# Performance work log

Measured on AMD Instinct MI355X. Metric: run time of the kernel, lower is better.

Reference implementation:

```python
import jax, jax.numpy as jnp
import numpy as np

B, S, D, H = 4, 2048, 1024, 16
HD = D // H  # head_size = 64
SCALE = HD ** -0.5


def setup_inputs() -> dict:
    key = jax.random.key(0)
    k1, k2, k3 = jax.random.split(key, 3)
    hidden_states = jax.random.normal(k1, (B, S, D), dtype=jnp.float32)
    W_qkv = jax.random.normal(k2, (D, 3 * D), dtype=jnp.float32) * 0.02
    W_out = jax.random.normal(k3, (D, D), dtype=jnp.float32) * 0.02
    return {"hidden_states": hidden_states, "W_qkv": W_qkv, "W_out": W_out}


def reference(hidden_states, W_qkv, W_out):
    b, s, d = hidden_states.shape
    qkv = hidden_states @ W_qkv                      # [b, s, 3d]
    q, k, v = jnp.split(qkv, 3, axis=-1)
    # [b, s, d] -> [b, H, s, hd]
    q = q.reshape(b, s, H, HD).transpose(0, 2, 1, 3)
    k = k.reshape(b, s, H, HD).transpose(0, 2, 1, 3)
    v = v.reshape(b, s, H, HD).transpose(0, 2, 1, 3)
    scores = jnp.einsum("bhqd,bhkd->bhqk", q, k) * SCALE  # [b, H, s, s]
    probs = jax.nn.softmax(scores, axis=-1)
    ctx = jnp.einsum("bhqk,bhkd->bhqd", probs, v)         # [b, H, s, hd]
    ctx = ctx.transpose(0, 2, 1, 3).reshape(b, s, d)
    out = ctx @ W_out
    return out
```

## Files before the change

kernel.cpp:

```cpp
#include <hip/hip_runtime.h>

typedef __attribute__((ext_vector_type(8))) __bf16 bf8;
typedef __attribute__((ext_vector_type(4))) float f4;
typedef __attribute__((ext_vector_type(8))) unsigned short us8;
typedef __attribute__((ext_vector_type(4))) unsigned short us4;
typedef __attribute__((ext_vector_type(4))) unsigned int u32x4;
typedef __attribute__((ext_vector_type(2))) unsigned int u32x2;

#define MFMA16(a, b, c) __builtin_amdgcn_mfma_f32_16x16x32_bf16((a), (b), (c), 0, 0, 0)
#define GLOAD16(gp, lp)                                                        \
  __builtin_amdgcn_global_load_lds(                                            \
      (const __attribute__((address_space(1))) void*)(gp),                     \
      (__attribute__((address_space(3))) void*)(lp), 16, 0, 0)

__device__ __forceinline__ unsigned short f2bf(float f) {
  unsigned u = __builtin_bit_cast(unsigned, f);
  u += 0x7FFFu + ((u >> 16) & 1u);
  return (unsigned short)(u >> 16);
}

__device__ __forceinline__ float fexp2(float x) {
  float r;
  asm("v_exp_f32 %0, %1" : "=v"(r) : "v"(x));
  return r;
}

__device__ __forceinline__ unsigned cvtpk(float a, float b) {
  unsigned r;
  asm("v_cvt_pk_bf16_f32 %0, %1, %2" : "=v"(r) : "v"(a), "v"(b));
  return r;
}

__global__ __launch_bounds__(256) void c_cast(const float* __restrict__ in,
                                              unsigned short* __restrict__ out) {
  int i = blockIdx.x * 256 + threadIdx.x;
  const float4* p = reinterpret_cast<const float4*>(in) + (size_t)i * 2;
  float4 a = p[0], b = p[1];
  us8 o;
  o[0] = f2bf(a.x); o[1] = f2bf(a.y); o[2] = f2bf(a.z); o[3] = f2bf(a.w);
  o[4] = f2bf(b.x); o[5] = f2bf(b.y); o[6] = f2bf(b.z); o[7] = f2bf(b.w);
  *reinterpret_cast<us8*>(&out[(size_t)i * 8]) = o;
}

__global__ __launch_bounds__(256) void c_trans(const float* __restrict__ in,
                                               unsigned short* __restrict__ out,
                                               int R, int C) {
  __shared__ float T[64][65];
  const int t = threadIdx.x;
  const int c0 = blockIdx.x * 64, r0 = blockIdx.y * 64;
  const int tr = t >> 4, tc = (t & 15) * 4;
#pragma unroll
  for (int i = 0; i < 4; ++i) {
    int r = tr + i * 16;
    float4 v = *reinterpret_cast<const float4*>(&in[(size_t)(r0 + r) * C + c0 + tc]);
    T[r][tc] = v.x; T[r][tc + 1] = v.y; T[r][tc + 2] = v.z; T[r][tc + 3] = v.w;
  }
  __syncthreads();
#pragma unroll
  for (int i = 0; i < 4; ++i) {
    int c = tr + i * 16;
    us4 o;
    o[0] = f2bf(T[tc + 0][c]); o[1] = f2bf(T[tc + 1][c]);
    o[2] = f2bf(T[tc + 2][c]); o[3] = f2bf(T[tc + 3][c]);
    *reinterpret_cast<us4*>(&out[(size_t)(c0 + c) * R + r0 + tc]) = o;
  }
}

__global__ __launch_bounds__(256) void k_qkv(const unsigned short* __restrict__ A,
                                             const unsigned short* __restrict__ Bt,
                                             unsigned short* __restrict__ Qo,
                                             unsigned short* __restrict__ Ko,
                                             unsigned short* __restrict__ Vo) {
  __shared__ unsigned short As[2][128 * 32];
  __shared__ unsigned short Bs[2][128 * 32];
  const int t = threadIdx.x;
  const int lane = t & 63, wid = t >> 6;
  const int wr = wid >> 1, wc = wid & 1;
  const int cl = lane & 15, kr8 = (lane >> 4) << 3;
  const int id = blockIdx.x;
  const int s = (id & 7) * 192 + (id >> 3);
  const int m0 = (s / 24) << 7, n0 = (s % 24) << 7;

  f4 acc[4][4];
#pragma unroll
  for (int i = 0; i < 4; ++i)
#pragma unroll
    for (int j = 0; j < 4; ++j) acc[i][j] = (f4){0.f, 0.f, 0.f, 0.f};

  auto STAGE = [&](int buf, int kt) {
    int k0 = kt << 5;
#pragma unroll
    for (int it = 0; it < 2; ++it) {
      int c = t + (it << 8);
      int wb = (t & 192) + (it << 8);
      GLOAD16(A + (size_t)(m0 + (c >> 2)) * 1024 + k0 + ((c & 3) << 3),
              (char*)As[buf] + (size_t)wb * 16);
      GLOAD16(Bt + (size_t)(n0 + (c >> 2)) * 1024 + k0 + ((c & 3) << 3),
              (char*)Bs[buf] + (size_t)wb * 16);
    }
  };

  STAGE(0, 0);
  __syncthreads();
  for (int kt = 0; kt < 32; ++kt) {
    int cur = kt & 1;
    if (kt < 31) STAGE(cur ^ 1, kt + 1);
    const unsigned short* as = As[cur];
    const unsigned short* bs = Bs[cur];
    bf8 af[4], bfr[4];
#pragma unroll
    for (int mi = 0; mi < 4; ++mi)
      af[mi] = *reinterpret_cast<const bf8*>(&as[(wr * 64 + mi * 16 + cl) * 32 + kr8]);
#pragma unroll
    for (int ni = 0; ni < 4; ++ni)
      bfr[ni] = *reinterpret_cast<const bf8*>(&bs[(wc * 64 + ni * 16 + cl) * 32 + kr8]);
#pragma unroll
    for (int mi = 0; mi < 4; ++mi)
#pragma unroll
      for (int ni = 0; ni < 4; ++ni)
        acc[mi][ni] = MFMA16(af[mi], bfr[ni], acc[mi][ni]);
    __syncthreads();
  }

#pragma unroll
  for (int mi = 0; mi < 4; ++mi) {
#pragma unroll
    for (int ni = 0; ni < 4; ++ni) {
      int gcol = n0 + wc * 64 + ni * 16 + cl;
      int grow0 = m0 + wr * 64 + mi * 16 + ((lane >> 4) << 2);
      int b = grow0 >> 11, s0 = grow0 & 2047;
      if (gcol < 1024) {
        int h = gcol >> 6, hd = gcol & 63;
#pragma unroll
        for (int r = 0; r < 4; ++r)
          Qo[((size_t)(b * 16 + h) * 2048 + s0 + r) * 64 + hd] =
              f2bf(acc[mi][ni][r] * 0.18033688011112042f);
      } else if (gcol < 2048) {
        int cc = gcol - 1024;
        int h = cc >> 6, hd = cc & 63;
#pragma unroll
        for (int r = 0; r < 4; ++r)
          Ko[((size_t)(b * 16 + h) * 2048 + s0 + r) * 64 + hd] = f2bf(acc[mi][ni][r]);
      } else {
        int cc = gcol - 2048;
        int h = cc >> 6, hd = cc & 63;
        us4 o;
        o[0] = f2bf(acc[mi][ni][0]); o[1] = f2bf(acc[mi][ni][1]);
        o[2] = f2bf(acc[mi][ni][2]); o[3] = f2bf(acc[mi][ni][3]);
        *reinterpret_cast<us4*>(&Vo[((size_t)(b * 16 + h) * 64 + hd) * 2048 + s0]) = o;
      }
    }
  }
}

__global__ __launch_bounds__(512) void k_attn(const unsigned short* __restrict__ Q,
                                              const unsigned short* __restrict__ K,
                                              const unsigned short* __restrict__ Vt,
                                              unsigned short* __restrict__ Ctx) {
  __shared__ __align__(16) unsigned short SMEM[2][2][64 * 64];
  __shared__ float RedS[128];
  const int t = threadIdx.x;
  const int lane = t & 63, wid = t >> 6;
  const int cl = lane & 15, g = lane >> 4;
  const int qg = wid >> 1, kg = wid & 1;
  const int id = blockIdx.x;
  const int sw = (id & 7) * 128 + (id >> 3);
  const int bh = sw >> 4, qb = sw & 15;
  const int b = bh >> 4, h = bh & 15;
  const int q0 = qb << 7;
  const size_t base = (size_t)bh * (2048 * 64);

  bf8 qf[2][2];
#pragma unroll
  for (int qi = 0; qi < 2; ++qi) {
    int qrow = q0 + qg * 32 + qi * 16 + cl;
    qf[qi][0] = *reinterpret_cast<const bf8*>(&Q[base + (size_t)qrow * 64 + (g << 3)]);
    qf[qi][1] = *reinterpret_cast<const bf8*>(&Q[base + (size_t)qrow * 64 + 32 + (g << 3)]);
  }

  const unsigned ones_u = 0x3F803F80u;
  u32x4 ones4 = (u32x4){ones_u, ones_u, ones_u, ones_u};
  bf8 onesb = __builtin_bit_cast(bf8, ones4);
  const f4 minit = (f4){-12.f, -12.f, -12.f, -12.f};

  f4 o[2][4], osum[2];
#pragma unroll
  for (int qi = 0; qi < 2; ++qi) {
#pragma unroll
    for (int n = 0; n < 4; ++n) o[qi][n] = (f4){0.f, 0.f, 0.f, 0.f};
    osum[qi] = (f4){0.f, 0.f, 0.f, 0.f};
  }

  auto STAGEK = [&](int buf, int kv0) {
    int kvl = t >> 3;
    int dblk = (t & 7) ^ (kvl & 7);
    GLOAD16(K + base + (size_t)(kv0 + kvl) * 64 + (dblk << 3),
            (char*)SMEM[0][buf] + (size_t)(t & 448) * 16);
  };
  auto STAGEV = [&](int buf, int kv0) {
    int d = t >> 3, ch = t & 7;
    int kq = ch ^ ((d >> 1) & 7);
    GLOAD16(Vt + base + (size_t)d * 2048 + kv0 + (kq << 3),
            (char*)SMEM[1][buf] + (size_t)(t & 448) * 16);
  };

  STAGEK(0, 0);
  STAGEV(0, 0);
  __syncthreads();

  for (int tk = 0; tk < 32; ++tk) {
    int cur = tk & 1;
    if (tk < 31) {
      STAGEK(cur ^ 1, (tk + 1) << 6);
      STAGEV(cur ^ 1, (tk + 1) << 6);
    }
    const char* kp = (const char*)SMEM[0][cur];
    const char* vp = (const char*)SMEM[1][cur];

    f4 sT[2][2];
    __builtin_amdgcn_s_setprio(1);
#pragma unroll
    for (int cb = 0; cb < 2; ++cb) {
      int row = (2 * kg + cb) * 16 + cl;
      bf8 a0 = *reinterpret_cast<const bf8*>(kp + row * 128 + ((g ^ (cl & 7)) << 4));
      bf8 a1 = *reinterpret_cast<const bf8*>(kp + row * 128 + (((4 + g) ^ (cl & 7)) << 4));
#pragma unroll
      for (int qi = 0; qi < 2; ++qi) {
        f4 s = minit;
        s = MFMA16(a0, qf[qi][0], s);
        s = MFMA16(a1, qf[qi][1], s);
        sT[cb][qi] = s;
      }
    }
    __builtin_amdgcn_s_setprio(0);

    u32x4 pw[2];
#pragma unroll
    for (int qi = 0; qi < 2; ++qi) {
      pw[qi][0] = cvtpk(fexp2(sT[0][qi][0]), fexp2(sT[0][qi][1]));
      pw[qi][1] = cvtpk(fexp2(sT[0][qi][2]), fexp2(sT[0][qi][3]));
      pw[qi][2] = cvtpk(fexp2(sT[1][qi][0]), fexp2(sT[1][qi][1]));
      pw[qi][3] = cvtpk(fexp2(sT[1][qi][2]), fexp2(sT[1][qi][3]));
    }
    bf8 pa0 = __builtin_bit_cast(bf8, pw[0]);
    bf8 pa1 = __builtin_bit_cast(bf8, pw[1]);

    const int q1 = 8 * kg + g, q2 = 8 * kg + 4 + g;
    unsigned vb = (unsigned)(cl * 128);
    unsigned o1 = (unsigned)((q1 ^ (cl & 14)) << 3);
    unsigned o2 = (unsigned)((q2 ^ (cl & 14)) << 3);
    __builtin_amdgcn_s_setprio(1);
#pragma unroll
    for (int n = 0; n < 4; ++n) {
      unsigned a = vb + (unsigned)(n * 2048);
      u32x2 lo = *reinterpret_cast<const u32x2*>(vp + a + o1);
      u32x2 hi = *reinterpret_cast<const u32x2*>(vp + a + o2);
      u32x4 bw = (u32x4){lo[0], lo[1], hi[0], hi[1]};
      bf8 vb8 = __builtin_bit_cast(bf8, bw);
      o[0][n] = MFMA16(pa0, vb8, o[0][n]);
      o[1][n] = MFMA16(pa1, vb8, o[1][n]);
    }
    osum[0] = MFMA16(pa0, onesb, osum[0]);
    osum[1] = MFMA16(pa1, onesb, osum[1]);
    __builtin_amdgcn_s_setprio(0);

    __syncthreads();
  }

  float* red = (float*)SMEM;
  if (kg) {
#pragma unroll
    for (int qi = 0; qi < 2; ++qi) {
#pragma unroll
      for (int n = 0; n < 4; ++n) {
        int ridx = qg * 8 + qi * 4 + n;
        *reinterpret_cast<f4*>(red + ridx * 256 + cl * 16 + g * 4) = o[qi][n];
      }
      if (cl == 0)
        *reinterpret_cast<f4*>(&RedS[(qg * 2 + qi) * 16 + g * 4]) = osum[qi];
    }
  }
  __syncthreads();
  if (!kg) {
#pragma unroll
    for (int qi = 0; qi < 2; ++qi) {
#pragma unroll
      for (int n = 0; n < 4; ++n) {
        int ridx = qg * 8 + qi * 4 + n;
        f4 po = *reinterpret_cast<const f4*>(red + ridx * 256 + cl * 16 + g * 4);
        o[qi][n] += po;
      }
      f4 ps = *reinterpret_cast<const f4*>(&RedS[(qg * 2 + qi) * 16 + g * 4]);
      osum[qi] += ps;
#pragma unroll
      for (int r = 0; r < 4; ++r) {
        float inv = 1.0f / osum[qi][r];
        int s = q0 + qg * 32 + qi * 16 + (g << 2) + r;
        size_t rb = ((size_t)b * 2048 + s) * 1024 + h * 64;
#pragma unroll
        for (int n = 0; n < 4; ++n) Ctx[rb + n * 16 + cl] = f2bf(o[qi][n][r] * inv);
      }
    }
  }
}

__global__ __launch_bounds__(256) void k_oproj(const unsigned short* __restrict__ A,
                                               const unsigned short* __restrict__ Bt,
                                               float* __restrict__ Out) {
  __shared__ unsigned short As[2][128 * 32];
  __shared__ unsigned short Bs[2][128 * 32];
  const int t = threadIdx.x;
  const int lane = t & 63, wid = t >> 6;
  const int wr = wid >> 1, wc = wid & 1;
  const int cl = lane & 15, kr8 = (lane >> 4) << 3;
  const int id = blockIdx.x;
  const int s = (id & 7) * 64 + (id >> 3);
  const int m0 = (s >> 3) << 7, n0 = (s & 7) << 7;

  f4 acc[4][4];
#pragma unroll
  for (int i = 0; i < 4; ++i)
#pragma unroll
    for (int j = 0; j < 4; ++j) acc[i][j] = (f4){0.f, 0.f, 0.f, 0.f};

  auto STAGE = [&](int buf, int kt) {
    int k0 = kt << 5;
#pragma unroll
    for (int it = 0; it < 2; ++it) {
      int c = t + (it << 8);
      int wb = (t & 192) + (it << 8);
      GLOAD16(A + (size_t)(m0 + (c >> 2)) * 1024 + k0 + ((c & 3) << 3),
              (char*)As[buf] + (size_t)wb * 16);
      GLOAD16(Bt + (size_t)(n0 + (c >> 2)) * 1024 + k0 + ((c & 3) << 3),
              (char*)Bs[buf] + (size_t)wb * 16);
    }
  };

  STAGE(0, 0);
  __syncthreads();
  for (int kt = 0; kt < 32; ++kt) {
    int cur = kt & 1;
    if (kt < 31) STAGE(cur ^ 1, kt + 1);
    const unsigned short* as = As[cur];
    const unsigned short* bs = Bs[cur];
    bf8 af[4], bfr[4];
#pragma unroll
    for (int mi = 0; mi < 4; ++mi)
      af[mi] = *reinterpret_cast<const bf8*>(&as[(wr * 64 + mi * 16 + cl) * 32 + kr8]);
#pragma unroll
    for (int ni = 0; ni < 4; ++ni)
      bfr[ni] = *reinterpret_cast<const bf8*>(&bs[(wc * 64 + ni * 16 + cl) * 32 + kr8]);
#pragma unroll
    for (int mi = 0; mi < 4; ++mi)
#pragma unroll
      for (int ni = 0; ni < 4; ++ni)
        acc[mi][ni] = MFMA16(af[mi], bfr[ni], acc[mi][ni]);
    __syncthreads();
  }

#pragma unroll
  for (int mi = 0; mi < 4; ++mi) {
#pragma unroll
    for (int ni = 0; ni < 4; ++ni) {
      int gcol = n0 + wc * 64 + ni * 16 + cl;
#pragma unroll
      for (int r = 0; r < 4; ++r) {
        int grow = m0 + wr * 64 + mi * 16 + ((lane >> 4) << 2) + r;
        Out[(size_t)grow * 1024 + gcol] = acc[mi][ni][r];
      }
    }
  }
}

extern "C" void kernel_launch(void* const* d_in, const int* in_sizes, int n_in,
                              void* d_out, int out_size, void* d_ws, size_t ws_size,
                              hipStream_t stream) {
  const float* hs = (const float*)d_in[0];
  const float* wqkv = (const float*)d_in[1];
  const float* wout = (const float*)d_in[2];
  float* out = (float*)d_out;

  unsigned short* ws = (unsigned short*)d_ws;
  const size_t NHS = (size_t)8192 * 1024;
  const size_t NWQ = (size_t)1024 * 3072;
  const size_t NWO = (size_t)1024 * 1024;
  const size_t NQ = (size_t)64 * 2048 * 64;

  unsigned short* hsb = ws;
  unsigned short* wqt = ws + NHS;
  unsigned short* wot = wqt + NWQ;
  unsigned short* Qw = wot + NWO;
  unsigned short* Kw = Qw + NQ;
  unsigned short* Vw = Kw + NQ;
  unsigned short* Cw = hsb;

  c_cast<<<dim3(4096), 256, 0, stream>>>(hs, hsb);
  c_trans<<<dim3(48, 16), 256, 0, stream>>>(wqkv, wqt, 1024, 3072);
  c_trans<<<dim3(16, 16), 256, 0, stream>>>(wout, wot, 1024, 1024);
  k_qkv<<<dim3(1536), 256, 0, stream>>>(hsb, wqt, Qw, Kw, Vw);
  k_attn<<<dim3(1024), 512, 0, stream>>>(Qw, Kw, Vw, Cw);
  k_oproj<<<dim3(512), 256, 0, stream>>>(Cw, wot, out);
}
```

Before: 195.1 us.

## Fuse prep kernels into one launch and deepen attention KV pipeline to four stages

Merges the hidden-state cast and the two weight transposes into a single c_prep launch that dispatches on block index, which removes two kernel launches. The attention kernel moves from a 2-slot to a 4-slot LDS ring and processes two KV tiles per iteration with one barrier, so loads are issued two tiles ahead and the number of __syncthreads is halved. This doubles LDS use for K/V tiles, which may lower occupancy, and the loop now contains two unrolled compute bodies, adding register pressure.

```diff
diff --git a/kernel.cpp b/kernel.cpp
--- a/kernel.cpp
+++ b/kernel.cpp
@@ -31,23 +31,32 @@
   return r;
 }
 
-__global__ __launch_bounds__(256) void c_cast(const float* __restrict__ in,
-                                              unsigned short* __restrict__ out) {
-  int i = blockIdx.x * 256 + threadIdx.x;
-  const float4* p = reinterpret_cast<const float4*>(in) + (size_t)i * 2;
-  float4 a = p[0], b = p[1];
-  us8 o;
-  o[0] = f2bf(a.x); o[1] = f2bf(a.y); o[2] = f2bf(a.z); o[3] = f2bf(a.w);
-  o[4] = f2bf(b.x); o[5] = f2bf(b.y); o[6] = f2bf(b.z); o[7] = f2bf(b.w);
-  *reinterpret_cast<us8*>(&out[(size_t)i * 8]) = o;
-}
-
-__global__ __launch_bounds__(256) void c_trans(const float* __restrict__ in,
-                                               unsigned short* __restrict__ out,
-                                               int R, int C) {
+__global__ __launch_bounds__(256) void c_prep(const float* __restrict__ hs,
+                                              unsigned short* __restrict__ hsb,
+                                              const float* __restrict__ wqkv,
+                                              unsigned short* __restrict__ wqt,
+                                              const float* __restrict__ wout,
+                                              unsigned short* __restrict__ wot) {
   __shared__ float T[64][65];
+  const int bid = blockIdx.x;
   const int t = threadIdx.x;
-  const int c0 = blockIdx.x * 64, r0 = blockIdx.y * 64;
+  if (bid < 4096) {
+    int i = bid * 256 + t;
+    const float4* p = reinterpret_cast<const float4*>(hs) + (size_t)i * 2;
+    float4 a = p[0], b = p[1];
+    us8 o;
+    o[0] = f2bf(a.x); o[1] = f2bf(a.y); o[2] = f2bf(a.z); o[3] = f2bf(a.w);
+    o[4] = f2bf(b.x); o[5] = f2bf(b.y); o[6] = f2bf(b.z); o[7] = f2bf(b.w);
+    *reinterpret_cast<us8*>(&hsb[(size_t)i * 8]) = o;
+    return;
+  }
+  const float* in;
+  unsigned short* out;
+  int R = 1024, C, idx;
+  if (bid < 4864) { idx = bid - 4096; in = wqkv; out = wqt; C = 3072; }
+  else            { idx = bid - 4864; in = wout; out = wot; C = 1024; }
+  const int nbc = C >> 6;
+  const int c0 = (idx % nbc) * 64, r0 = (idx / nbc) * 64;
   const int tr = t >> 4, tc = (t & 15) * 4;
 #pragma unroll
   for (int i = 0; i < 4; ++i) {
@@ -157,7 +166,7 @@
                                               const unsigned short* __restrict__ K,
                                               const unsigned short* __restrict__ Vt,
                                               unsigned short* __restrict__ Ctx) {
-  __shared__ __align__(16) unsigned short SMEM[2][2][64 * 64];
+  __shared__ __align__(16) unsigned short SMEM[4][2][64 * 64];
   __shared__ float RedS[128];
   const int t = threadIdx.x;
   const int lane = t & 63, wid = t >> 6;
@@ -191,32 +200,20 @@
     osum[qi] = (f4){0.f, 0.f, 0.f, 0.f};
   }
 
-  auto STAGEK = [&](int buf, int kv0) {
+  auto STAGEK = [&](int slot, int kv0) {
     int kvl = t >> 3;
     int dblk = (t & 7) ^ (kvl & 7);
     GLOAD16(K + base + (size_t)(kv0 + kvl) * 64 + (dblk << 3),
-            (char*)SMEM[0][buf] + (size_t)(t & 448) * 16);
+            (char*)SMEM[slot][0] + (size_t)(t & 448) * 16);
   };
-  auto STAGEV = [&](int buf, int kv0) {
+  auto STAGEV = [&](int slot, int kv0) {
     int d = t >> 3, ch = t & 7;
     int kq = ch ^ ((d >> 1) & 7);
     GLOAD16(Vt + base + (size_t)d * 2048 + kv0 + (kq << 3),
-            (char*)SMEM[1][buf] + (size_t)(t & 448) * 16);
+            (char*)SMEM[slot][1] + (size_t)(t & 448) * 16);
   };
 
-  STAGEK(0, 0);
-  STAGEV(0, 0);
-  __syncthreads();
-
-  for (int tk = 0; tk < 32; ++tk) {
-    int cur = tk & 1;
-    if (tk < 31) {
-      STAGEK(cur ^ 1, (tk + 1) << 6);
-      STAGEV(cur ^ 1, (tk + 1) << 6);
-    }
-    const char* kp = (const char*)SMEM[0][cur];
-    const char* vp = (const char*)SMEM[1][cur];
-
+  auto COMPUTE = [&](const char* kp, const char* vp) {
     f4 sT[2][2];
     __builtin_amdgcn_s_setprio(1);
 #pragma unroll
@@ -263,7 +260,24 @@
     osum[0] = MFMA16(pa0, onesb, osum[0]);
     osum[1] = MFMA16(pa1, onesb, osum[1]);
     __builtin_amdgcn_s_setprio(0);
-
+  };
+
+  STAGEK(0, 0);
+  STAGEV(0, 0);
+  STAGEK(1, 64);
+  STAGEV(1, 64);
+  __syncthreads();
+
+  for (int ti = 0; ti < 16; ++ti) {
+    int t0 = 2 * ti, t1 = t0 + 1;
+    if (ti < 15) {
+      STAGEK((t0 + 2) & 3, (t0 + 2) << 6);
+      STAGEV((t0 + 2) & 3, (t0 + 2) << 6);
+      STAGEK((t1 + 2) & 3, (t1 + 2) << 6);
+      STAGEV((t1 + 2) & 3, (t1 + 2) << 6);
+    }
+    COMPUTE((const char*)SMEM[t0 & 3][0], (const char*)SMEM[t0 & 3][1]);
+    COMPUTE((const char*)SMEM[t1 & 3][0], (const char*)SMEM[t1 & 3][1]);
     __syncthreads();
   }
 
@@ -394,9 +408,7 @@
   unsigned short* Vw = Kw + NQ;
   unsigned short* Cw = hsb;
 
-  c_cast<<<dim3(4096), 256, 0, stream>>>(hs, hsb);
-  c_trans<<<dim3(48, 16), 256, 0, stream>>>(wqkv, wqt, 1024, 3072);
-  c_trans<<<dim3(16, 16), 256, 0, stream>>>(wout, wot, 1024, 1024);
+  c_prep<<<dim3(5120), 256, 0, stream>>>(hs, hsb, wqkv, wqt, wout, wot);
   k_qkv<<<dim3(1536), 256, 0, stream>>>(hsb, wqt, Qw, Kw, Vw);
   k_attn<<<dim3(1024), 512, 0, stream>>>(Qw, Kw, Vw, Cw);
   k_oproj<<<dim3(512), 256, 0, stream>>>(Cw, wot, out);
```

After: 186.7 us. -4.3%, faster.
